# Kernel optimization log

Measured on AMD Instinct MI355X. Metric: run time of the kernel, lower is better.

## Reference

```python
import jax, jax.numpy as jnp
import numpy as np

STRIDE, PAD, DIL = 1, 1, 1
KH, KW = 3, 3


def setup_inputs() -> dict:
    key = jax.random.key(0)
    k1, k2, k3 = jax.random.split(key, 3)
    N, C, H, W = 8, 64, 128, 128
    O = 64
    x = jax.random.normal(k1, (N, C, H, W), dtype=jnp.float32)
    # offset layout: [N, deformable_groups*2*KH*KW, H_out, W_out], (y,x) interleaved per kernel tap
    offset = jax.random.normal(k2, (N, 2 * KH * KW, H, W), dtype=jnp.float32)
    stdv = 1.0 / np.sqrt(C * KH * KW)
    weight = jax.random.uniform(k3, (O, C, KH, KW), dtype=jnp.float32, minval=-stdv, maxval=stdv)
    return {"x": x, "offset": offset, "weight": weight}


def _deform_conv2d(x, offset, weight):
    N, C, H, W = x.shape
    O = weight.shape[0]
    Ho = (H + 2 * PAD - (DIL * (KH - 1) + 1)) // STRIDE + 1
    Wo = (W + 2 * PAD - (DIL * (KW - 1) + 1)) // STRIDE + 1
    K = KH * KW

    # offsets: [N, KH, KW, 2, Ho, Wo] -> (dy, dx) per kernel tap
    off = offset.reshape(N, KH, KW, 2, Ho, Wo)
    oy, ox = off[:, :, :, 0], off[:, :, :, 1]  # [N,KH,KW,Ho,Wo]

    base_y = (jnp.arange(Ho, dtype=jnp.float32) * STRIDE - PAD)  # [Ho]
    base_x = (jnp.arange(Wo, dtype=jnp.float32) * STRIDE - PAD)  # [Wo]
    ky = jnp.arange(KH, dtype=jnp.float32) * DIL
    kx = jnp.arange(KW, dtype=jnp.float32) * DIL

    # fractional sampling positions [N,KH,KW,Ho,Wo]
    py = base_y[None, None, None, :, None] + ky[None, :, None, None, None] + oy
    px = base_x[None, None, None, None, :] + kx[None, None, :, None, None] + ox

    y0f = jnp.floor(py)
    x0f = jnp.floor(px)
    wy = py - y0f  # bilinear weights
    wx = px - x0f
    y0 = y0f.astype(jnp.int32)
    x0 = x0f.astype(jnp.int32)

    x_flat = x.reshape(N, C, H * W)

    def gather(yi, xi):
        # zero-padded bilinear corner gather -> [N, C, K*Ho*Wo]
        valid = ((yi >= 0) & (yi < H) & (xi >= 0) & (xi < W)).reshape(N, 1, -1)
        yc = jnp.clip(yi, 0, H - 1)
        xc = jnp.clip(xi, 0, W - 1)
        idx = (yc * W + xc).reshape(N, 1, -1)
        v = jnp.take_along_axis(x_flat, idx, axis=2)
        return v * valid.astype(x.dtype)

    wy_f = wy.reshape(N, 1, -1)
    wx_f = wx.reshape(N, 1, -1)
    sampled = (
        gather(y0, x0) * (1.0 - wy_f) * (1.0 - wx_f)
        + gather(y0, x0 + 1) * (1.0 - wy_f) * wx_f
        + gather(y0 + 1, x0) * wy_f * (1.0 - wx_f)
        + gather(y0 + 1, x0 + 1) * wy_f * wx_f
    )  # [N, C, K*Ho*Wo]

    sampled = sampled.reshape(N, C, K, Ho * Wo)
    out = jnp.einsum("nckp,ock->nop", sampled, weight.reshape(O, C, K))
    return out.reshape(N, O, Ho, Wo)


def reference(x, offset, weight):
    return _deform_conv2d(x, offset, weight)
```

## Files before the change

kernel.cpp:

```cpp
#include <hip/hip_runtime.h>

#define H_ 128
#define W_ 128
#define HW 16384
#define C_ 64
#define O_ 64
#define N_ 8

typedef __attribute__((ext_vector_type(4))) float f32x4;
typedef __attribute__((ext_vector_type(2))) _Float16 f16x2;
typedef __attribute__((ext_vector_type(8))) _Float16 f16x8;

__device__ __forceinline__ unsigned short f2h(float f) {
    union { _Float16 h; unsigned short u; } c;
    c.h = (_Float16)f;
    return c.u;
}

__global__ __launch_bounds__(256) void prep_all(const float* __restrict__ x,
                                                const float* __restrict__ off,
                                                const float* __restrict__ w,
                                                unsigned short* __restrict__ xt,
                                                unsigned short* __restrict__ bp,
                                                unsigned* __restrict__ metap,
                                                unsigned* __restrict__ w01p,
                                                unsigned* __restrict__ w23p) {
    __shared__ unsigned short tile[32][65];
    const int bid = blockIdx.x;
    const int tid = threadIdx.x;

    if (bid < 4096) {
        const int n = bid & 7;
        const int rest = bid >> 3;
        const int wt = rest & 3, h = rest >> 2;
        const int w0 = wt * 32;
        const int wl = tid & 31, cg = tid >> 5;
#pragma unroll
        for (int r = 0; r < 8; ++r) {
            const int c = cg * 8 + r;
            const float v = x[(((size_t)(n * 64 + c) * 128 + h) * 128) + w0 + wl];
            tile[wl][c] = f2h(v);
        }
        __syncthreads();
        const int c2 = tid & 63, wg = tid >> 6;
#pragma unroll
        for (int r = 0; r < 8; ++r) {
            const int ww = wg * 8 + r;
            xt[(((size_t)(n * 128 + h) * 128 + w0 + ww) << 6) + c2] = tile[ww][c2];
        }
    } else if (bid < 8704) {
        const int lbid = bid - 4096;
        const int n = lbid & 7;
        const int rem = lbid >> 3;
        const int j = rem >> 6;
        const int pix = ((rem & 63) << 8) + tid;
        const int kh = j / 3, kw = j - kh * 3;
        const int ho = pix >> 7, wo = pix & 127;

        const float* ob = off + (size_t)(n * 18 + 2 * j) * HW + pix;
        const float oy = ob[0];
        const float ox = ob[HW];
        const float py = (float)(ho - 1 + kh) + oy;
        const float px = (float)(wo - 1 + kw) + ox;
        const float y0f = floorf(py), x0f = floorf(px);
        const float wy = py - y0f, wx = px - x0f;
        const int y0 = (int)y0f, x0 = (int)x0f;
        const bool vy0 = (unsigned)y0 < 128u;
        const bool vy1 = (unsigned)(y0 + 1) < 128u;
        const bool vx0 = (unsigned)x0 < 128u;
        const bool vx1 = (unsigned)(x0 + 1) < 128u;
        const int y0c = min(max(y0, 0), 127), y1c = min(max(y0 + 1, 0), 127);
        const int x0c = min(max(x0, 0), 127), x1c = min(max(x0 + 1, 0), 127);
        const float s00 = (1.f - wy) * (1.f - wx) * ((vy0 & vx0) ? 1.f : 0.f);
        const float s01 = (1.f - wy) * wx * ((vy0 & vx1) ? 1.f : 0.f);
        const float s10 = wy * (1.f - wx) * ((vy1 & vx0) ? 1.f : 0.f);
        const float s11 = wy * wx * ((vy1 & vx1) ? 1.f : 0.f);

        const int t = ho & ~7, tx0 = wo & ~15;
        const int sy0 = y0c - t + 6, sy1 = y1c - t + 6;
        const int sx0 = x0c - tx0 + 6, sx1 = x1c - tx0 + 6;
        const bool ok = ((unsigned)sy0 <= 19u) & ((unsigned)sy1 <= 19u) &
                        ((unsigned)sx0 <= 27u) & ((unsigned)sx1 <= 27u);
        unsigned meta;
        if (ok) {
            const unsigned k00 = ((unsigned)(sy0 * 28 + sx0) << 2) | (unsigned)(sx0 & 3);
            meta = 0x80000000u | k00 | ((unsigned)(x1c - x0c) << 12) | ((unsigned)(y1c - y0c) << 13);
        } else {
            meta = ((unsigned)(y0c * 128 + x0c) << 16) | ((unsigned)(x1c - x0c) << 1) | (unsigned)(y1c - y0c);
        }
        const size_t e = (size_t)(n * 9 + j) * HW + pix;
        metap[e] = meta;
        w01p[e] = (unsigned)f2h(s00) | ((unsigned)f2h(s01) << 16);
        w23p[e] = (unsigned)f2h(s10) | ((unsigned)f2h(s11) << 16);
    } else {
        const int idx = (bid - 8704) * 256 + tid;
        if (idx < 36864) {
            const int i = idx & 7;
            const int lane = (idx >> 3) & 63;
            const int ot = (idx >> 9) & 3;
            const int h = (idx >> 11) & 1;
            const int j = idx >> 12;
            const int o = ot * 16 + (lane & 15);
            const int c = h * 32 + (lane >> 4) * 8 + i;
            bp[idx] = f2h(w[(o * 64 + c) * 9 + j]);
        }
    }
}

__global__ __launch_bounds__(256, 4) void dcn_mfma(const unsigned short* __restrict__ xt,
                                                   const unsigned* __restrict__ metap,
                                                   const unsigned* __restrict__ w01p,
                                                   const unsigned* __restrict__ w23p,
                                                   const unsigned short* __restrict__ bp,
                                                   float* __restrict__ out) {
    __shared__ uint4 lds4[2240];

    const int tid = threadIdx.x;
    const int lane = tid & 63;
    const int wid = tid >> 6;
    const int lrow = lane & 15;
    const int lgrp = lane >> 4;

    const int bid = blockIdx.x;
    const int n = bid & 7;
    const int tile = bid >> 3;
    const int t   = (tile >> 3) << 3;
    const int tx0 = (tile & 7) << 4;

    const unsigned short* xn = xt + (size_t)n * (HW * 64);
    const unsigned char* xb = (const unsigned char*)xn;
    const f16x8* bg = (const f16x8*)bp;
    const size_t nplane = (size_t)n * 9 * HW;
    const unsigned* mp  = metap + nplane;
    const unsigned* wpa = w01p + nplane;
    const unsigned* wpb = w23p + nplane;

    f32x4 acc[2][4];
#pragma unroll
    for (int q = 0; q < 2; ++q)
#pragma unroll
        for (int r = 0; r < 4; ++r) acc[q][r] = (f32x4){0.f, 0.f, 0.f, 0.f};

#pragma unroll 1
    for (int h = 0; h < 2; ++h) {
        if (h) __syncthreads();
        for (int c = tid; c < 560; c += 256) {
            const int ry = c / 28, rx = c - ry * 28;
            const int gy = min(max(t - 6 + ry, 0), 127);
            const int gx = min(max(tx0 - 6 + rx, 0), 127);
            const uint4* src = (const uint4*)(xn + ((((gy << 7) + gx) << 6) | (h << 5)));
            const int d = c << 2, sw = rx & 3;
#pragma unroll
            for (int sub = 0; sub < 4; ++sub) lds4[d + (sub ^ sw)] = src[sub];
        }
        __syncthreads();

#pragma unroll
        for (int q = 0; q < 2; ++q) {
            const int ho = t + (wid << 1) + q;
            const int pixb = (ho << 7) + tx0 + lrow;

#pragma unroll 3
            for (int j = 0; j < 9; ++j) {
                const int e = j * HW + pixb;
                const unsigned meta = mp[e];
                const unsigned wab = wpa[e];
                const unsigned wcd = wpb[e];
                union { unsigned u; f16x2 h2; } W00, W01, W10, W11;
                W00.u = __builtin_amdgcn_perm(wab, wab, 0x01000100u);
                W01.u = __builtin_amdgcn_perm(wab, wab, 0x03020302u);
                W10.u = __builtin_amdgcn_perm(wcd, wcd, 0x01000100u);
                W11.u = __builtin_amdgcn_perm(wcd, wcd, 0x03020302u);

                const bool ok = (int)meta < 0;
                const unsigned k00 = meta & 0xfffu;
                const unsigned dx = (meta >> 12) & 1u;
                const unsigned k01 = ((k00 & ~3u) + (dx << 2)) | (((k00 & 3u) + dx) & 3u);
                const unsigned dyi = (meta & 0x2000u) ? 112u : 0u;
                const unsigned k10 = k00 + dyi, k11 = k01 + dyi;

                uint4 T00 = lds4[k00 ^ (unsigned)lgrp];
                uint4 T01 = lds4[k01 ^ (unsigned)lgrp];
                uint4 T10 = lds4[k10 ^ (unsigned)lgrp];
                uint4 T11 = lds4[k11 ^ (unsigned)lgrp];
                if (!__all(ok)) {
                    if (!ok) {
                        const unsigned gpos = (meta >> 16) & 0x3fffu;
                        const int dxo = (int)((meta >> 1) & 1u) << 7;
                        const int dyo = (int)(meta & 1u) << 14;
                        const unsigned char* p = xb + ((gpos << 7) | (h << 6)) + (lgrp << 4);
                        T00 = *(const uint4*)p;
                        T01 = *(const uint4*)(p + dxo);
                        T10 = *(const uint4*)(p + dyo);
                        T11 = *(const uint4*)(p + dyo + dxo);
                    }
                }
                union { uint4 u; f16x2 h2[4]; f16x8 v; } A, U00, U01, U10, U11;
                U00.u = T00; U01.u = T01; U10.u = T10; U11.u = T11;
#pragma unroll
                for (int k = 0; k < 4; ++k)
                    A.h2[k] = U00.h2[k] * W00.h2 + U01.h2[k] * W01.h2
                            + U10.h2[k] * W10.h2 + U11.h2[k] * W11.h2;
                const int fb = ((j * 2 + h) << 8) + lane;
                acc[q][0] = __builtin_amdgcn_mfma_f32_16x16x32_f16(A.v, bg[fb],       acc[q][0], 0, 0, 0);
                acc[q][1] = __builtin_amdgcn_mfma_f32_16x16x32_f16(A.v, bg[fb + 64],  acc[q][1], 0, 0, 0);
                acc[q][2] = __builtin_amdgcn_mfma_f32_16x16x32_f16(A.v, bg[fb + 128], acc[q][2], 0, 0, 0);
                acc[q][3] = __builtin_amdgcn_mfma_f32_16x16x32_f16(A.v, bg[fb + 192], acc[q][3], 0, 0, 0);
            }
        }
    }

#pragma unroll
    for (int q = 0; q < 2; ++q) {
        float* opb = out + (size_t)n * (O_ * HW) + ((t + (wid << 1) + q) << 7) + tx0 + lgrp * 4;
        *(f32x4*)(opb + (size_t)(0 * 16 + lrow) * HW) = acc[q][0];
        *(f32x4*)(opb + (size_t)(1 * 16 + lrow) * HW) = acc[q][1];
        *(f32x4*)(opb + (size_t)(2 * 16 + lrow) * HW) = acc[q][2];
        *(f32x4*)(opb + (size_t)(3 * 16 + lrow) * HW) = acc[q][3];
    }
}

extern "C" void kernel_launch(void* const* d_in, const int* in_sizes, int n_in,
                              void* d_out, int out_size, void* d_ws, size_t ws_size,
                              hipStream_t stream) {
    const float* x = (const float*)d_in[0];
    const float* off = (const float*)d_in[1];
    const float* w = (const float*)d_in[2];
    float* out = (float*)d_out;

    char* ws = (char*)d_ws;
    unsigned short* bp = (unsigned short*)ws;
    unsigned short* xt = (unsigned short*)(ws + 73728);
    unsigned* metap = (unsigned*)(ws + 16850944);
    unsigned* w01p  = (unsigned*)(ws + 21569536);
    unsigned* w23p  = (unsigned*)(ws + 26288128);

    prep_all<<<8848, 256, 0, stream>>>(x, off, w, xt, bp, metap, w01p, w23p);
    dcn_mfma<<<1024, 256, 0, stream>>>(xt, metap, w01p, w23p, bp, out);
}
```

Before: 57.51 us.

## Stage full 64-channel halo tile in LDS once, one row per wave

New measurement: 60.08 us. 4.5% more time.

```diff
diff --git a/kernel.cpp b/kernel.cpp
--- a/kernel.cpp
+++ b/kernel.cpp
@@ -107,13 +107,13 @@
     }
 }
 
-__global__ __launch_bounds__(256, 4) void dcn_mfma(const unsigned short* __restrict__ xt,
+__global__ __launch_bounds__(512, 4) void dcn_mfma(const unsigned short* __restrict__ xt,
                                                    const unsigned* __restrict__ metap,
                                                    const unsigned* __restrict__ w01p,
                                                    const unsigned* __restrict__ w23p,
                                                    const unsigned short* __restrict__ bp,
                                                    float* __restrict__ out) {
-    __shared__ uint4 lds4[2240];
+    __shared__ uint4 lds4[5600];
 
     const int tid = threadIdx.x;
     const int lane = tid & 63;
@@ -135,89 +135,91 @@
     const unsigned* wpa = w01p + nplane;
     const unsigned* wpb = w23p + nplane;
 
-    f32x4 acc[2][4];
-#pragma unroll
-    for (int q = 0; q < 2; ++q)
-#pragma unroll
-        for (int r = 0; r < 4; ++r) acc[q][r] = (f32x4){0.f, 0.f, 0.f, 0.f};
-
-#pragma unroll 1
-    for (int h = 0; h < 2; ++h) {
-        if (h) __syncthreads();
-        for (int c = tid; c < 560; c += 256) {
-            const int ry = c / 28, rx = c - ry * 28;
-            const int gy = min(max(t - 6 + ry, 0), 127);
-            const int gx = min(max(tx0 - 6 + rx, 0), 127);
-            const uint4* src = (const uint4*)(xn + ((((gy << 7) + gx) << 6) | (h << 5)));
-            const int d = c << 2, sw = rx & 3;
-#pragma unroll
-            for (int sub = 0; sub < 4; ++sub) lds4[d + (sub ^ sw)] = src[sub];
-        }
-        __syncthreads();
-
-#pragma unroll
-        for (int q = 0; q < 2; ++q) {
-            const int ho = t + (wid << 1) + q;
-            const int pixb = (ho << 7) + tx0 + lrow;
+    for (int i = tid; i < 4480; i += 512) {
+        const int pos = i >> 3, sub = i & 7;
+        const int ry = pos / 28, rx = pos - ry * 28;
+        const int gy = min(max(t - 6 + ry, 0), 127);
+        const int gx = min(max(tx0 - 6 + rx, 0), 127);
+        const uint4* src = (const uint4*)(xn + (((gy << 7) + gx) << 6));
+        lds4[(pos << 3) + (sub ^ (rx & 3))] = src[sub];
+    }
+    __syncthreads();
+
+    const int ho = t + wid;
+    const int pixb = (ho << 7) + tx0 + lrow;
+
+    f32x4 acc[4];
+#pragma unroll
+    for (int r = 0; r < 4; ++r) acc[r] = (f32x4){0.f, 0.f, 0.f, 0.f};
 
 #pragma unroll 3
-            for (int j = 0; j < 9; ++j) {
-                const int e = j * HW + pixb;
-                const unsigned meta = mp[e];
-                const unsigned wab = wpa[e];
-                const unsigned wcd = wpb[e];
-                union { unsigned u; f16x2 h2; } W00, W01, W10, W11;
-                W00.u = __builtin_amdgcn_perm(wab, wab, 0x01000100u);
-                W01.u = __builtin_amdgcn_perm(wab, wab, 0x03020302u);
-                W10.u = __builtin_amdgcn_perm(wcd, wcd, 0x01000100u);
-                W11.u = __builtin_amdgcn_perm(wcd, wcd, 0x03020302u);
-
-                const bool ok = (int)meta < 0;
-                const unsigned k00 = meta & 0xfffu;
-                const unsigned dx = (meta >> 12) & 1u;
-                const unsigned k01 = ((k00 & ~3u) + (dx << 2)) | (((k00 & 3u) + dx) & 3u);
-                const unsigned dyi = (meta & 0x2000u) ? 112u : 0u;
-                const unsigned k10 = k00 + dyi, k11 = k01 + dyi;
-
-                uint4 T00 = lds4[k00 ^ (unsigned)lgrp];
-                uint4 T01 = lds4[k01 ^ (unsigned)lgrp];
-                uint4 T10 = lds4[k10 ^ (unsigned)lgrp];
-                uint4 T11 = lds4[k11 ^ (unsigned)lgrp];
-                if (!__all(ok)) {
-                    if (!ok) {
-                        const unsigned gpos = (meta >> 16) & 0x3fffu;
-                        const int dxo = (int)((meta >> 1) & 1u) << 7;
-                        const int dyo = (int)(meta & 1u) << 14;
-                        const unsigned char* p = xb + ((gpos << 7) | (h << 6)) + (lgrp << 4);
-                        T00 = *(const uint4*)p;
-                        T01 = *(const uint4*)(p + dxo);
-                        T10 = *(const uint4*)(p + dyo);
-                        T11 = *(const uint4*)(p + dyo + dxo);
-                    }
-                }
-                union { uint4 u; f16x2 h2[4]; f16x8 v; } A, U00, U01, U10, U11;
-                U00.u = T00; U01.u = T01; U10.u = T10; U11.u = T11;
-#pragma unroll
-                for (int k = 0; k < 4; ++k)
-                    A.h2[k] = U00.h2[k] * W00.h2 + U01.h2[k] * W01.h2
-                            + U10.h2[k] * W10.h2 + U11.h2[k] * W11.h2;
-                const int fb = ((j * 2 + h) << 8) + lane;
-                acc[q][0] = __builtin_amdgcn_mfma_f32_16x16x32_f16(A.v, bg[fb],       acc[q][0], 0, 0, 0);
-                acc[q][1] = __builtin_amdgcn_mfma_f32_16x16x32_f16(A.v, bg[fb + 64],  acc[q][1], 0, 0, 0);
-                acc[q][2] = __builtin_amdgcn_mfma_f32_16x16x32_f16(A.v, bg[fb + 128], acc[q][2], 0, 0, 0);
-                acc[q][3] = __builtin_amdgcn_mfma_f32_16x16x32_f16(A.v, bg[fb + 192], acc[q][3], 0, 0, 0);
+    for (int j = 0; j < 9; ++j) {
+        const int e = j * HW + pixb;
+        const unsigned meta = mp[e];
+        const unsigned wab = wpa[e];
+        const unsigned wcd = wpb[e];
+        union { unsigned u; f16x2 h2; } W00, W01, W10, W11;
+        W00.u = __builtin_amdgcn_perm(wab, wab, 0x01000100u);
+        W01.u = __builtin_amdgcn_perm(wab, wab, 0x03020302u);
+        W10.u = __builtin_amdgcn_perm(wcd, wcd, 0x01000100u);
+        W11.u = __builtin_amdgcn_perm(wcd, wcd, 0x03020302u);
+
+        const bool ok = (int)meta < 0;
+        const unsigned k00 = meta & 0xfffu;
+        const unsigned dx = (meta >> 12) & 1u;
+        const unsigned k01 = ((k00 & ~3u) + (dx << 2)) | (((k00 & 3u) + dx) & 3u);
+        const unsigned dyi = (meta & 0x2000u) ? 112u : 0u;
+        const unsigned k10 = k00 + dyi, k11 = k01 + dyi;
+        const unsigned b00 = ((k00 & ~3u) << 1) + ((unsigned)lgrp ^ (k00 & 3u));
+        const unsigned b01 = ((k01 & ~3u) << 1) + ((unsigned)lgrp ^ (k01 & 3u));
+        const unsigned b10 = ((k10 & ~3u) << 1) + ((unsigned)lgrp ^ (k10 & 3u));
+        const unsigned b11 = ((k11 & ~3u) << 1) + ((unsigned)lgrp ^ (k11 & 3u));
+
+        uint4 T00a = lds4[b00],     T01a = lds4[b01],     T10a = lds4[b10],     T11a = lds4[b11];
+        uint4 T00b = lds4[b00 + 4], T01b = lds4[b01 + 4], T10b = lds4[b10 + 4], T11b = lds4[b11 + 4];
+        if (!__all(ok)) {
+            if (!ok) {
+                const unsigned gpos = (meta >> 16) & 0x3fffu;
+                const int dxo = (int)((meta >> 1) & 1u) << 7;
+                const int dyo = (int)(meta & 1u) << 14;
+                const unsigned char* p = xb + (gpos << 7) + (lgrp << 4);
+                T00a = *(const uint4*)p;              T00b = *(const uint4*)(p + 64);
+                T01a = *(const uint4*)(p + dxo);      T01b = *(const uint4*)(p + dxo + 64);
+                T10a = *(const uint4*)(p + dyo);      T10b = *(const uint4*)(p + dyo + 64);
+                T11a = *(const uint4*)(p + dyo + dxo);T11b = *(const uint4*)(p + dyo + dxo + 64);
             }
         }
+        const int fb0 = ((j * 2) << 8) + lane;
+        {
+            union { uint4 u; f16x2 h2[4]; f16x8 v; } A, U00, U01, U10, U11;
+            U00.u = T00a; U01.u = T01a; U10.u = T10a; U11.u = T11a;
+#pragma unroll
+            for (int k = 0; k < 4; ++k)
+                A.h2[k] = U00.h2[k] * W00.h2 + U01.h2[k] * W01.h2
+                        + U10.h2[k] * W10.h2 + U11.h2[k] * W11.h2;
+            acc[0] = __builtin_amdgcn_mfma_f32_16x16x32_f16(A.v, bg[fb0],       acc[0], 0, 0, 0);
+            acc[1] = __builtin_amdgcn_mfma_f32_16x16x32_f16(A.v, bg[fb0 + 64],  acc[1], 0, 0, 0);
+            acc[2] = __builtin_amdgcn_mfma_f32_16x16x32_f16(A.v, bg[fb0 + 128], acc[2], 0, 0, 0);
+            acc[3] = __builtin_amdgcn_mfma_f32_16x16x32_f16(A.v, bg[fb0 + 192], acc[3], 0, 0, 0);
+        }
+        {
+            union { uint4 u; f16x2 h2[4]; f16x8 v; } A, U00, U01, U10, U11;
+            U00.u = T00b; U01.u = T01b; U10.u = T10b; U11.u = T11b;
+#pragma unroll
+            for (int k = 0; k < 4; ++k)
+                A.h2[k] = U00.h2[k] * W00.h2 + U01.h2[k] * W01.h2
+                        + U10.h2[k] * W10.h2 + U11.h2[k] * W11.h2;
+            acc[0] = __builtin_amdgcn_mfma_f32_16x16x32_f16(A.v, bg[fb0 + 256], acc[0], 0, 0, 0);
+            acc[1] = __builtin_amdgcn_mfma_f32_16x16x32_f16(A.v, bg[fb0 + 320], acc[1], 0, 0, 0);
+            acc[2] = __builtin_amdgcn_mfma_f32_16x16x32_f16(A.v, bg[fb0 + 384], acc[2], 0, 0, 0);
+            acc[3] = __builtin_amdgcn_mfma_f32_16x16x32_f16(A.v, bg[fb0 + 448], acc[3], 0, 0, 0);
+        }
     }
 
-#pragma unroll
-    for (int q = 0; q < 2; ++q) {
-        float* opb = out + (size_t)n * (O_ * HW) + ((t + (wid << 1) + q) << 7) + tx0 + lgrp * 4;
-        *(f32x4*)(opb + (size_t)(0 * 16 + lrow) * HW) = acc[q][0];
-        *(f32x4*)(opb + (size_t)(1 * 16 + lrow) * HW) = acc[q][1];
-        *(f32x4*)(opb + (size_t)(2 * 16 + lrow) * HW) = acc[q][2];
-        *(f32x4*)(opb + (size_t)(3 * 16 + lrow) * HW) = acc[q][3];
-    }
+    float* opb = out + (size_t)n * (O_ * HW) + ((size_t)ho << 7) + tx0 + lgrp * 4;
+#pragma unroll
+    for (int qq = 0; qq < 4; ++qq)
+        *(f32x4*)(opb + (size_t)(qq * 16 + lrow) * HW) = acc[qq];
 }
 
 extern "C" void kernel_launch(void* const* d_in, const int* in_sizes, int n_in,
@@ -236,5 +238,5 @@
     unsigned* w23p  = (unsigned*)(ws + 26288128);
 
     prep_all<<<8848, 256, 0, stream>>>(x, off, w, xt, bp, metap, w01p, w23p);
-    dcn_mfma<<<1024, 256, 0, stream>>>(xt, metap, w01p, w23p, bp, out);
-}
+    dcn_mfma<<<1024, 512, 0, stream>>>(xt, metap, w01p, w23p, bp, out);
+}
```
